# Optimization experiments

Hardware: AMD Instinct MI355X
Metric: run time of the kernel (lower is better)

## Reference

```python
import jax, jax.numpy as jnp
import numpy as np

B, T, D, V, SPK = 8, 4096, 512, 1024, 512
DECAY = 0.95
COARSE_SCALE = 0.2
RES_SCALE = 0.35
MAX_LS = 1.2
MAX_SIL = 0.35
COLD_RUNS = 2.0
MIN_DUR = 2.0


def gelu(x):
    return jax.nn.gelu(x, approximate=False)


def setup_inputs() -> dict:
    key = jax.random.key(0)
    ks = jax.random.split(key, 24)
    def n(k, shape, s=1.0):
        return jax.random.normal(k, shape, dtype=jnp.float32) * s
    inp = {}
    inp['content_units'] = jax.random.randint(ks[0], (B, T), 0, V)
    inp['log_anchor'] = n(ks[1], (B, T), 0.5) + 1.0
    inp['unit_mask'] = jax.random.randint(ks[2], (B, T), 0, 2)
    inp['sealed_mask'] = jax.random.randint(ks[3], (B, T), 0, 2)
    inp['silence_mask'] = jax.random.randint(ks[4], (B, T), 0, 2)
    inp['sep_hint'] = jax.random.uniform(ks[5], (B, T), dtype=jnp.float32)
    inp['edge_cue'] = jax.random.uniform(ks[6], (B, T), dtype=jnp.float32)
    inp['run_stability'] = jax.random.uniform(ks[7], (B, T), dtype=jnp.float32)
    inp['global_rate'] = n(ks[8], (B,), 0.1) + 1.0
    inp['local_rate_ema'] = n(ks[9], (B, 1), 0.1) + 1.0
    inp['spk_embed'] = n(ks[10], (B, SPK))
    s = 0.02
    inp['emb_table'] = n(ks[11], (V, D), s)
    inp['feat_W'] = n(ks[12], (5, D), s)      # scalar features -> dim
    inp['feat_b'] = jnp.zeros((D,), jnp.float32)
    inp['spk_W'] = n(ks[13], (SPK, D), s)
    inp['spk_b'] = jnp.zeros((D,), jnp.float32)
    inp['coarse_W1'] = n(ks[14], (D + 1, D), s)
    inp['coarse_b1'] = jnp.zeros((D,), jnp.float32)
    inp['coarse_W2'] = n(ks[15], (D, 1), s)
    inp['coarse_b2'] = jnp.zeros((1,), jnp.float32)
    inp['res_W1'] = n(ks[16], (2 * D + 1, D), s)
    inp['res_b1'] = jnp.zeros((D,), jnp.float32)
    inp['res_W2'] = n(ks[17], (D, 1), s)
    inp['res_b2'] = jnp.zeros((1,), jnp.float32)
    inp['src_rate_init'] = jnp.zeros((1,), jnp.float32)
    return inp


def _local_rate_scan(observed_log, speech_mask, init_rate):
    # Causal masked exponential-decay recurrence: emitted rate at t is the
    # state BEFORE observing step t (strictly causal); state only updates on
    # speech-commit steps.
    def step(rate, xs):
        obs, m = xs  # [B], [B]
        new = jnp.where(m > 0, DECAY * rate + (1.0 - DECAY) * obs, rate)
        return new, rate
    final, seq = jax.lax.scan(step, init_rate, (observed_log.T, speech_mask.T))
    return seq.T, final[:, None]  # [B,T], [B,1]


def reference(content_units, log_anchor, unit_mask, sealed_mask, silence_mask,
              sep_hint, edge_cue, run_stability, global_rate, local_rate_ema,
              spk_embed, emb_table, feat_W, feat_b, spk_W, spk_b,
              coarse_W1, coarse_b1, coarse_W2, coarse_b2,
              res_W1, res_b1, res_W2, res_b2, src_rate_init):
    f32 = jnp.float32
    mask = jnp.clip(unit_mask.astype(f32), 0.0, 1.0)
    sealed = jnp.clip(sealed_mask.astype(f32), 0.0, 1.0)
    silence = jnp.clip(silence_mask.astype(f32), 0.0, 1.0) * mask
    stability = jnp.clip(run_stability.astype(f32), 0.0, 1.0) * mask
    commit = mask * sealed
    sil_commit = commit * silence
    speech = commit * (1.0 - silence)

    la = log_anchor.astype(f32)
    rate_seq, rate_final = _local_rate_scan(la, speech, local_rate_ema[:, 0].astype(f32))

    # CausalUnitRunEncoder: token embedding + projection of per-step scalars
    feats = jnp.stack([la, rate_seq, silence, sep_hint.astype(f32), edge_cue.astype(f32)], axis=-1)  # [B,T,5]
    query = gelu(emb_table[content_units] + feats @ feat_W + feat_b) * mask[..., None]  # [B,T,D]

    grc = global_rate.astype(f32).reshape(-1, 1)[:, :1]  # [B,1]
    spk_ctx = jnp.tanh(spk_embed.astype(f32) @ spk_W + spk_b)  # [B,D]

    gsa = (grc - rate_seq) * commit  # global_shift_analytic [B,T]
    coarse_in = jnp.concatenate([spk_ctx, grc], axis=-1)  # [B,D+1]
    coarse_scalar = COARSE_SCALE * jnp.tanh((gelu(coarse_in @ coarse_W1 + coarse_b1) @ coarse_W2 + coarse_b2)[:, 0])  # [B]
    coarse_corr = coarse_scalar[:, None] * commit
    global_term = (gsa + coarse_corr) * commit

    # residual head: split first-layer weights to avoid materializing the concat
    Wq, Ws, wg = res_W1[:D], res_W1[D:2 * D], res_W1[2 * D]
    h = gelu(query @ Wq + (spk_ctx @ Ws)[:, None, :] + global_term[..., None] * wg + res_b1)  # [B,T,D]
    residual = RES_SCALE * jnp.tanh((h @ res_W2 + res_b2)[..., 0])  # [B,T]

    prefix_prev = jnp.maximum(jnp.cumsum(speech, axis=1) - speech, 0.0)
    cold_gate = jnp.clip(prefix_prev / COLD_RUNS, 0.0, 1.0)
    short_gate = jnp.clip((jnp.maximum(jnp.exp(la), 1.0) - 1.0) / max(1.0, MIN_DUR - 1.0), 0.0, 1.0)
    residual_gate = cold_gate * short_gate * stability * speech
    residual = residual * residual_gate

    pred_speech = jnp.clip(global_term + residual, -MAX_LS, MAX_LS) * speech
    pred_silence = jnp.clip(global_term, -MAX_SIL, MAX_SIL) * sil_commit
    pred = pred_speech + pred_silence  # unit_logstretch [B,T]
    return pred
```

## Files before the change

kernel.cpp:

```cpp
#include <hip/hip_runtime.h>
#include <hip/hip_bf16.h>

#define BB 8
#define TT 4096
#define DD 512
#define MM (BB*TT)
#define DECAYF 0.95f
#define OMDECAYF (1.0f - 0.95f)

typedef __attribute__((ext_vector_type(8))) short bf16x8;
typedef __attribute__((ext_vector_type(4))) float f32x4;

__device__ __forceinline__ float gelu_f(float x){
  return 0.5f * x * (1.0f + erff(x * 0.70710678118654752f));
}

__device__ __forceinline__ unsigned f2bf(float x){
  unsigned u = __float_as_uint(x);
  return (u + 0x7FFFu + ((u >> 16) & 1u)) >> 16;
}

__global__ __launch_bounds__(512) void pre_kernel(
    const float* __restrict__ spk_embed, const float* __restrict__ spk_W,
    const float* __restrict__ spk_b, const float* __restrict__ rW1,
    const float* __restrict__ la_g, const int* __restrict__ um,
    const int* __restrict__ sm, const int* __restrict__ zm,
    const float* __restrict__ stab_g, const float* __restrict__ lre,
    float* __restrict__ spk_ctx, unsigned short* __restrict__ wqt,
    float* __restrict__ rate_seq, float* __restrict__ rgate_a,
    int* __restrict__ active_list, int* __restrict__ acount)
{
  __shared__ float se[DD];
  __shared__ float red[8][64];
  __shared__ float tile[64][65];
  __shared__ float wAg[8], wBg[8], wSg[8];
  __shared__ int wcnt[8];
  int blk = blockIdx.x, t = threadIdx.x;
  int lane = t & 63, wid = t >> 6;

  if (blk < 64){
    int b = blk >> 3, d0 = (blk & 7) * 64;
    int dl = lane, ks = wid;
    se[t] = spk_embed[b*DD + t];
    __syncthreads();
    float a = 0.f;
    const float* wp = spk_W + (long)(ks*64)*DD + d0 + dl;
    #pragma unroll 8
    for (int k = 0; k < 64; ++k) a += se[ks*64 + k] * wp[(long)k*DD];
    red[ks][dl] = a;
    __syncthreads();
    if (t < 64){
      float s = spk_b[d0 + t];
      #pragma unroll
      for (int i = 0; i < 8; ++i) s += red[i][t];
      spk_ctx[b*DD + d0 + t] = tanhf(s);
    }
    return;
  }
  if (blk < 128){
    int tb = blk - 64;
    int nb = (tb & 7) * 64, kb = (tb >> 3) * 64;
    int tx = t & 63, ty = t >> 6;
    #pragma unroll
    for (int i = 0; i < 8; ++i){
      int k = ty + i*8;
      tile[k][tx] = rW1[(long)(kb + k)*DD + nb + tx];
    }
    __syncthreads();
    #pragma unroll
    for (int i = 0; i < 8; ++i){
      int nl = ty + i*8;
      wqt[(long)(nb + nl)*DD + kb + tx] = (unsigned short)f2bf(tile[tx][nl]);
    }
    return;
  }

  int b = blk - 128;
  int base = b*TT + t*8;
  float4 la0 = *(const float4*)(la_g + base);
  float4 la1 = *(const float4*)(la_g + base + 4);
  int4 u0 = *(const int4*)(um + base), u1 = *(const int4*)(um + base + 4);
  int4 s0 = *(const int4*)(sm + base), s1 = *(const int4*)(sm + base + 4);
  int4 z0 = *(const int4*)(zm + base), z1 = *(const int4*)(zm + base + 4);
  float4 st0 = *(const float4*)(stab_g + base), st1 = *(const float4*)(stab_g + base + 4);
  float lav[8] = {la0.x,la0.y,la0.z,la0.w,la1.x,la1.y,la1.z,la1.w};
  int uv[8] = {u0.x,u0.y,u0.z,u0.w,u1.x,u1.y,u1.z,u1.w};
  int sv[8] = {s0.x,s0.y,s0.z,s0.w,s1.x,s1.y,s1.z,s1.w};
  int zv[8] = {z0.x,z0.y,z0.z,z0.w,z1.x,z1.y,z1.z,z1.w};
  float stv_[8] = {st0.x,st0.y,st0.z,st0.w,st1.x,st1.y,st1.z,st1.w};
  float spv[8], stv[8];

  float A = 1.f, Bv = 0.f, S = 0.f;
  #pragma unroll
  for (int i = 0; i < 8; ++i){
    float m = uv[i] > 0 ? 1.f : 0.f;
    float sealed = sv[i] > 0 ? 1.f : 0.f;
    float sil = (zv[i] > 0 ? 1.f : 0.f) * m;
    float speech = (m * sealed) * (1.f - sil);
    spv[i] = speech;
    stv[i] = fminf(fmaxf(stv_[i], 0.f), 1.f) * m;
    if (speech > 0.f){
      Bv = DECAYF*Bv + OMDECAYF*lav[i];
      A *= DECAYF;
      S += 1.f;
    }
  }
  #pragma unroll
  for (int d = 1; d < 64; d <<= 1){
    float Au = __shfl_up(A, d, 64);
    float Bu = __shfl_up(Bv, d, 64);
    float Su = __shfl_up(S, d, 64);
    if (lane >= d){ Bv = A*Bu + Bv; A = A*Au; S += Su; }
  }
  if (lane == 63){ wAg[wid] = A; wBg[wid] = Bv; wSg[wid] = S; }
  float Ale = __shfl_up(A, 1, 64), Ble = __shfl_up(Bv, 1, 64), Sle = __shfl_up(S, 1, 64);
  if (lane == 0){ Ale = 1.f; Ble = 0.f; Sle = 0.f; }
  __syncthreads();
  float Awp = 1.f, Bwp = 0.f, Swp = 0.f;
  for (int w = 0; w < wid; ++w){
    Bwp = wAg[w]*Bwp + wBg[w];
    Awp = wAg[w]*Awp;
    Swp += wSg[w];
  }
  float Bex = Ale*Bwp + Ble;
  float Aex = Ale*Awp;
  float Sex = Swp + Sle;

  float rate = Aex*lre[b] + Bex;
  float ps = Sex;
  float ro[8], rg[8];
  #pragma unroll
  for (int i = 0; i < 8; ++i){
    ro[i] = rate;
    float cold = fminf(ps * 0.5f, 1.f);
    float shortg = fminf(fmaxf(expf(lav[i]) - 1.f, 0.f), 1.f);
    rg[i] = cold * shortg * stv[i] * spv[i];
    if (spv[i] > 0.f){
      rate = DECAYF*rate + OMDECAYF*lav[i];
      ps += 1.f;
    }
  }
  *(float4*)(rate_seq + base)     = make_float4(ro[0],ro[1],ro[2],ro[3]);
  *(float4*)(rate_seq + base + 4) = make_float4(ro[4],ro[5],ro[6],ro[7]);
  *(float4*)(rgate_a + base)      = make_float4(rg[0],rg[1],rg[2],rg[3]);
  *(float4*)(rgate_a + base + 4)  = make_float4(rg[4],rg[5],rg[6],rg[7]);

  int nact = 0;
  #pragma unroll
  for (int i = 0; i < 8; ++i) nact += (rg[i] != 0.f) ? 1 : 0;
  int inc = nact;
  #pragma unroll
  for (int d = 1; d < 64; d <<= 1){
    int u = __shfl_up(inc, d, 64);
    if (lane >= d) inc += u;
  }
  int myex = inc - nact;
  if (lane == 63) wcnt[wid] = inc;
  __syncthreads();
  int wbase = 0;
  for (int w = 0; w < wid; ++w) wbase += wcnt[w];
  int pos = wbase + myex;
  int* alist = active_list + b*TT;
  #pragma unroll
  for (int i = 0; i < 8; ++i){
    if (rg[i] != 0.f) alist[pos++] = base + i;
  }
  if (t == 0){
    int total = 0;
    #pragma unroll
    for (int w = 0; w < 8; ++w) total += wcnt[w];
    acount[b] = total;
  }
}

__global__ __launch_bounds__(512) void prep2_kernel(
    const float* __restrict__ spk_ctx, const float* __restrict__ rW1,
    const float* __restrict__ cW1, const float* __restrict__ cb1,
    const float* __restrict__ cW2, const float* __restrict__ grate,
    float* __restrict__ s_vec, float* __restrict__ coarse_part)
{
  __shared__ float sc[DD];
  __shared__ float red1[8][64];
  __shared__ float red2[8][64];
  int blk = blockIdx.x;
  int b = blk >> 3, d0 = (blk & 7) * 64;
  int t = threadIdx.x, dl = t & 63, ks = t >> 6;
  sc[t] = spk_ctx[b*DD + t];
  __syncthreads();
  float a1 = 0.f, a2 = 0.f;
  const float* wsp = rW1 + (long)(DD + ks*64)*DD + d0 + dl;
  const float* wcp = cW1 + (long)(ks*64)*DD + d0 + dl;
  #pragma unroll 4
  for (int k = 0; k < 64; ++k){
    float s = sc[ks*64 + k];
    a1 += s * wsp[(long)k*DD];
    a2 += s * wcp[(long)k*DD];
  }
  red1[ks][dl] = a1; red2[ks][dl] = a2;
  __syncthreads();
  if (t < 64){
    int d = d0 + t;
    float s1 = 0.f;
    float s2 = cb1[d] + grate[b] * cW1[(long)DD*DD + d];
    #pragma unroll
    for (int i = 0; i < 8; ++i){ s1 += red1[i][t]; s2 += red2[i][t]; }
    s_vec[b*DD + d] = s1;
    float hv = gelu_f(s2) * cW2[d];
    #pragma unroll
    for (int sh = 1; sh < 64; sh <<= 1) hv += __shfl_xor(hv, sh, 64);
    if (t == 0) coarse_part[blk] = hv;
  }
}

__global__ __launch_bounds__(512) void main_kernel(
    const int* __restrict__ content, const float* __restrict__ la_g,
    const float* __restrict__ sep, const float* __restrict__ edge,
    const float* __restrict__ emb, const float* __restrict__ fW,
    const float* __restrict__ fb, const float* __restrict__ rate_seq,
    const unsigned short* __restrict__ wqt,
    const float* __restrict__ s_vec, const float* __restrict__ rW1,
    const float* __restrict__ rb1, const float* __restrict__ rW2,
    const float* __restrict__ rb2, const float* __restrict__ grate,
    const float* __restrict__ coarse_part, const float* __restrict__ cb2,
    const int* __restrict__ um, const int* __restrict__ sm,
    const int* __restrict__ zm,
    const float* __restrict__ rgate_a, const int* __restrict__ active_list,
    const int* __restrict__ acount, float* __restrict__ out)
{
  __shared__ unsigned short Af[16*32*32];
  __shared__ unsigned short Bs[2][512*32];
  __shared__ float part[8][32];
  __shared__ int seg_sh[3];
  int blk = blockIdx.x, tid = threadIdx.x, wid = tid >> 6, lane = tid & 63;

  if (tid < 128){
    int gr = blk*128 + tid;
    float rgv = rgate_a[gr];
    if (rgv == 0.f){
      int b = gr >> 12;
      float csum = cb2[0];
      #pragma unroll
      for (int c = 0; c < 8; ++c) csum += coarse_part[b*8 + c];
      float cs = 0.2f * tanhf(csum);
      float m = um[gr] > 0 ? 1.f : 0.f;
      float sealed = sm[gr] > 0 ? 1.f : 0.f;
      float sil = (zm[gr] > 0 ? 1.f : 0.f) * m;
      float commit = m * sealed;
      float speech = commit * (1.f - sil);
      float silc = commit * sil;
      float g = (grate[b] - rate_seq[gr] + cs) * commit;
      out[gr] = fminf(fmaxf(g, -1.2f), 1.2f) * speech
              + fminf(fmaxf(g, -0.35f), 0.35f) * silc;
    }
  }

  const char* wbase = (const char*)wqt;
  auto stageB = [&](unsigned short* dstbuf, int kc){
    int k0b = kc * 64;
    #pragma unroll
    for (int i = 0; i < 4; ++i){
      int j = wid*4 + i;
      int n = j*16 + (lane >> 2);
      int slot = (lane & 3) ^ ((n >> 1) & 3);
      const char* src = wbase + (long)n*1024 + k0b + slot*16;
      char* dst = (char*)dstbuf + j*1024 + (lane << 4);
      __builtin_amdgcn_global_load_lds(
          (const __attribute__((address_space(1))) void*)src,
          (__attribute__((address_space(3))) void*)dst, 16, 0, 0);
    }
  };

  for (int p = blk; ; p += 256){
    if (tid == 0){
      int cum = 0, sb = -1, slo = 0, scnt = 0;
      #pragma unroll
      for (int b = 0; b < BB; ++b){
        int c = acount[b];
        int nb = (c + 31) >> 5;
        if (sb < 0 && p < cum + nb){ sb = b; slo = (p - cum) * 32; scnt = c; }
        cum += nb;
      }
      seg_sh[0] = sb; seg_sh[1] = slo; seg_sh[2] = scnt;
    }
    __syncthreads();
    int seg_b = seg_sh[0], seg_lo = seg_sh[1], seg_cnt = seg_sh[2];
    if (seg_b < 0) break;
    const int* alist = active_list + seg_b*TT;

    float csum = cb2[0];
    #pragma unroll
    for (int c = 0; c < 8; ++c) csum += coarse_part[seg_b*8 + c];
    float cs = 0.2f * tanhf(csum);
    float grc = grate[seg_b];

    stageB(&Bs[0][0], 0);

    {
      int rr = tid >> 4, kc = tid & 15;
      int q = seg_lo + rr; if (q > seg_cnt-1) q = seg_cnt-1;
      int gr = alist[q];
      float la = la_g[gr], rate = rate_seq[gr];
      float sepv = sep[gr], edgev = edge[gr];
      int k0 = kc * 32;
      const float* er = emb + (long)content[gr]*DD + k0;
      int c = (rr >> 1) & 3;
      char* abase = (char*)Af + kc*2048 + rr*64;
      #pragma unroll
      for (int s2 = 0; s2 < 4; ++s2){
        int kk = k0 + s2*8;
        float4 e0 = *(const float4*)(er + s2*8);
        float4 e1 = *(const float4*)(er + s2*8 + 4);
        float4 w00 = *(const float4*)(fW + kk);
        float4 w01 = *(const float4*)(fW + kk + 4);
        float4 w10 = *(const float4*)(fW + DD + kk);
        float4 w11 = *(const float4*)(fW + DD + kk + 4);
        float4 w30 = *(const float4*)(fW + 3*DD + kk);
        float4 w31 = *(const float4*)(fW + 3*DD + kk + 4);
        float4 w40 = *(const float4*)(fW + 4*DD + kk);
        float4 w41 = *(const float4*)(fW + 4*DD + kk + 4);
        float4 b0 = *(const float4*)(fb + kk);
        float4 b1 = *(const float4*)(fb + kk + 4);
        unsigned v0 = f2bf(gelu_f(e0.x + la*w00.x + rate*w10.x + sepv*w30.x + edgev*w40.x + b0.x));
        unsigned v1 = f2bf(gelu_f(e0.y + la*w00.y + rate*w10.y + sepv*w30.y + edgev*w40.y + b0.y));
        unsigned v2 = f2bf(gelu_f(e0.z + la*w00.z + rate*w10.z + sepv*w30.z + edgev*w40.z + b0.z));
        unsigned v3 = f2bf(gelu_f(e0.w + la*w00.w + rate*w10.w + sepv*w30.w + edgev*w40.w + b0.w));
        unsigned v4 = f2bf(gelu_f(e1.x + la*w01.x + rate*w11.x + sepv*w31.x + edgev*w41.x + b1.x));
        unsigned v5 = f2bf(gelu_f(e1.y + la*w01.y + rate*w11.y + sepv*w31.y + edgev*w41.y + b1.y));
        unsigned v6 = f2bf(gelu_f(e1.z + la*w01.z + rate*w11.z + sepv*w31.z + edgev*w41.z + b1.z));
        unsigned v7 = f2bf(gelu_f(e1.w + la*w01.w + rate*w11.w + sepv*w31.w + edgev*w41.w + b1.w));
        int4 pkv = make_int4((int)((v1 << 16) | v0), (int)((v3 << 16) | v2),
                             (int)((v5 << 16) | v4), (int)((v7 << 16) | v6));
        *(int4*)(abase + ((s2 ^ c) << 4)) = pkv;
      }
    }
    __syncthreads();

    f32x4 acc[2][4];
    #pragma unroll
    for (int i = 0; i < 2; ++i)
      #pragma unroll
      for (int j = 0; j < 4; ++j) acc[i][j] = (f32x4){0.f,0.f,0.f,0.f};

    int rgp = lane >> 4, li = lane & 15;
    #pragma unroll
    for (int kc = 0; kc < 16; ++kc){
      if (kc < 15) stageB(&Bs[(kc+1)&1][0], kc+1);
      if (kc < 15) asm volatile("s_waitcnt vmcnt(4)" ::: "memory");
      else         asm volatile("s_waitcnt vmcnt(0)" ::: "memory");
      const char* bsb = (const char*)&Bs[kc&1][0];
      bf16x8 a[2], bb[4];
      #pragma unroll
      for (int mt = 0; mt < 2; ++mt){
        int row = mt*16 + li;
        int slot = rgp ^ ((row >> 1) & 3);
        a[mt] = *(const bf16x8*)((const char*)Af + kc*2048 + row*64 + (slot << 4));
      }
      #pragma unroll
      for (int nt = 0; nt < 4; ++nt){
        int n = wid*64 + nt*16 + li;
        int slot = rgp ^ ((n >> 1) & 3);
        bb[nt] = *(const bf16x8*)(bsb + n*64 + slot*16);
      }
      #pragma unroll
      for (int mt = 0; mt < 2; ++mt)
        #pragma unroll
        for (int nt = 0; nt < 4; ++nt)
          acc[mt][nt] = __builtin_amdgcn_mfma_f32_16x16x32_bf16(a[mt], bb[nt], acc[mt][nt], 0, 0, 0);
    }

    float svv[4], wgv[4], b1v[4], w2v[4];
    #pragma unroll
    for (int nt = 0; nt < 4; ++nt){
      int j = wid*64 + nt*16 + li;
      svv[nt] = s_vec[seg_b*DD + j];
      wgv[nt] = rW1[1024*DD + j];
      b1v[nt] = rb1[j];
      w2v[nt] = rW2[j];
    }
    #pragma unroll
    for (int mt = 0; mt < 2; ++mt){
      #pragma unroll
      for (int r = 0; r < 4; ++r){
        int row = mt*16 + rgp*4 + r;
        int q = seg_lo + row; if (q > seg_cnt-1) q = seg_cnt-1;
        int gr = alist[q];
        float gt = grc - rate_seq[gr] + cs;
        float s = 0.f;
        #pragma unroll
        for (int nt = 0; nt < 4; ++nt){
          float y = acc[mt][nt][r] + svv[nt] + gt*wgv[nt] + b1v[nt];
          s += gelu_f(y) * w2v[nt];
        }
        s += __shfl_xor(s, 1, 64);
        s += __shfl_xor(s, 2, 64);
        s += __shfl_xor(s, 4, 64);
        s += __shfl_xor(s, 8, 64);
        if (li == 0) part[wid][row] = s;
      }
    }
    __syncthreads();
    if (tid < 32){
      int q = seg_lo + tid;
      if (q < seg_cnt){
        int gr = alist[q];
        float s = 0.f;
        #pragma unroll
        for (int w = 0; w < 8; ++w) s += part[w][tid];
        float resid = 0.35f * tanhf(s + rb2[0]) * rgate_a[gr];
        float g = grc - rate_seq[gr] + cs;
        out[gr] = fminf(fmaxf(g + resid, -1.2f), 1.2f);
      }
    }
    __syncthreads();
  }
}

extern "C" void kernel_launch(void* const* d_in, const int* in_sizes, int n_in,
                              void* d_out, int out_size, void* d_ws, size_t ws_size,
                              hipStream_t stream)
{
  const int*   content = (const int*)  d_in[0];
  const float* la      = (const float*)d_in[1];
  const int*   um      = (const int*)  d_in[2];
  const int*   smk     = (const int*)  d_in[3];
  const int*   zm      = (const int*)  d_in[4];
  const float* sep     = (const float*)d_in[5];
  const float* edge    = (const float*)d_in[6];
  const float* stab    = (const float*)d_in[7];
  const float* grate   = (const float*)d_in[8];
  const float* lre     = (const float*)d_in[9];
  const float* spk_e   = (const float*)d_in[10];
  const float* emb     = (const float*)d_in[11];
  const float* fW      = (const float*)d_in[12];
  const float* fb      = (const float*)d_in[13];
  const float* spk_W   = (const float*)d_in[14];
  const float* spk_b   = (const float*)d_in[15];
  const float* cW1     = (const float*)d_in[16];
  const float* cb1     = (const float*)d_in[17];
  const float* cW2     = (const float*)d_in[18];
  const float* cb2     = (const float*)d_in[19];
  const float* rW1     = (const float*)d_in[20];
  const float* rb1     = (const float*)d_in[21];
  const float* rW2     = (const float*)d_in[22];
  const float* rb2     = (const float*)d_in[23];

  char* w = (char*)d_ws;
  unsigned short* wsWqT = (unsigned short*)(w);
  size_t off = 524288;
  float* rate_seq = (float*)(w + off); off += MM*4;
  float* rgate_a  = (float*)(w + off); off += MM*4;
  int*   active_list = (int*)(w + off); off += MM*4;
  float* s_vec    = (float*)(w + off); off += BB*DD*4;
  float* spk_ctx  = (float*)(w + off); off += BB*DD*4;
  float* coarse_part = (float*)(w + off); off += 64*4;
  int*   acount   = (int*)(w + off); off += 256;

  pre_kernel<<<136, 512, 0, stream>>>(spk_e, spk_W, spk_b, rW1,
      la, um, smk, zm, stab, lre,
      spk_ctx, wsWqT, rate_seq, rgate_a, active_list, acount);
  prep2_kernel<<<64, 512, 0, stream>>>(spk_ctx, rW1, cW1, cb1, cW2, grate,
                                       s_vec, coarse_part);
  main_kernel<<<256, 512, 0, stream>>>(content, la, sep, edge, emb, fW, fb,
      rate_seq, wsWqT, s_vec, rW1, rb1, rW2, rb2, grate, coarse_part, cb2,
      um, smk, zm, rgate_a, active_list, acount, (float*)d_out);
}
```

Baseline: 41.58 us.

## Precompute query activations in mid kernel and stream them into LDS via global_load_lds

Moves the embedding+feature GELU query computation out of the GEMM main kernel into the former prep2 kernel, now a 576-block mid_kernel that writes bf16 query rows for active tokens to a 32MB workspace. The main kernel then loads its A tile straight into LDS with global_load_lds and no longer does the gather and GELU in its prologue. The aim is to take the prologue latency off the GEMM blocks and spread it over more parallel blocks. The cost is an extra write and read of up to 32MB of bf16 activations through global memory.

```diff
diff --git a/kernel.cpp b/kernel.cpp
--- a/kernel.cpp
+++ b/kernel.cpp
@@ -173,50 +173,88 @@
   }
 }
 
-__global__ __launch_bounds__(512) void prep2_kernel(
+__global__ __launch_bounds__(512) void mid_kernel(
     const float* __restrict__ spk_ctx, const float* __restrict__ rW1,
     const float* __restrict__ cW1, const float* __restrict__ cb1,
     const float* __restrict__ cW2, const float* __restrict__ grate,
-    float* __restrict__ s_vec, float* __restrict__ coarse_part)
-{
-  __shared__ float sc[DD];
-  __shared__ float red1[8][64];
-  __shared__ float red2[8][64];
-  int blk = blockIdx.x;
-  int b = blk >> 3, d0 = (blk & 7) * 64;
-  int t = threadIdx.x, dl = t & 63, ks = t >> 6;
-  sc[t] = spk_ctx[b*DD + t];
-  __syncthreads();
-  float a1 = 0.f, a2 = 0.f;
-  const float* wsp = rW1 + (long)(DD + ks*64)*DD + d0 + dl;
-  const float* wcp = cW1 + (long)(ks*64)*DD + d0 + dl;
-  #pragma unroll 4
-  for (int k = 0; k < 64; ++k){
-    float s = sc[ks*64 + k];
-    a1 += s * wsp[(long)k*DD];
-    a2 += s * wcp[(long)k*DD];
-  }
-  red1[ks][dl] = a1; red2[ks][dl] = a2;
-  __syncthreads();
-  if (t < 64){
-    int d = d0 + t;
-    float s1 = 0.f;
-    float s2 = cb1[d] + grate[b] * cW1[(long)DD*DD + d];
-    #pragma unroll
-    for (int i = 0; i < 8; ++i){ s1 += red1[i][t]; s2 += red2[i][t]; }
-    s_vec[b*DD + d] = s1;
-    float hv = gelu_f(s2) * cW2[d];
-    #pragma unroll
-    for (int sh = 1; sh < 64; sh <<= 1) hv += __shfl_xor(hv, sh, 64);
-    if (t == 0) coarse_part[blk] = hv;
-  }
-}
-
-__global__ __launch_bounds__(512) void main_kernel(
     const int* __restrict__ content, const float* __restrict__ la_g,
     const float* __restrict__ sep, const float* __restrict__ edge,
     const float* __restrict__ emb, const float* __restrict__ fW,
     const float* __restrict__ fb, const float* __restrict__ rate_seq,
+    const int* __restrict__ active_list, const int* __restrict__ acount,
+    float* __restrict__ s_vec, float* __restrict__ coarse_part,
+    unsigned short* __restrict__ wsQ)
+{
+  int blk = blockIdx.x, t = threadIdx.x;
+  int lane = t & 63, wid = t >> 6;
+
+  if (blk < 64){
+    __shared__ float sc[DD];
+    __shared__ float red1[8][64];
+    __shared__ float red2[8][64];
+    int b = blk >> 3, d0 = (blk & 7) * 64;
+    int dl = lane, ks = wid;
+    sc[t] = spk_ctx[b*DD + t];
+    __syncthreads();
+    float a1 = 0.f, a2 = 0.f;
+    const float* wsp = rW1 + (long)(DD + ks*64)*DD + d0 + dl;
+    const float* wcp = cW1 + (long)(ks*64)*DD + d0 + dl;
+    #pragma unroll 4
+    for (int k = 0; k < 64; ++k){
+      float s = sc[ks*64 + k];
+      a1 += s * wsp[(long)k*DD];
+      a2 += s * wcp[(long)k*DD];
+    }
+    red1[ks][dl] = a1; red2[ks][dl] = a2;
+    __syncthreads();
+    if (t < 64){
+      int d = d0 + t;
+      float s1 = 0.f;
+      float s2 = cb1[d] + grate[b] * cW1[(long)DD*DD + d];
+      #pragma unroll
+      for (int i = 0; i < 8; ++i){ s1 += red1[i][t]; s2 += red2[i][t]; }
+      s_vec[b*DD + d] = s1;
+      float hv = gelu_f(s2) * cW2[d];
+      #pragma unroll
+      for (int sh = 1; sh < 64; sh <<= 1) hv += __shfl_xor(hv, sh, 64);
+      if (t == 0) coarse_part[blk] = hv;
+    }
+    return;
+  }
+
+  int tb = blk - 64;
+  int b = tb >> 6;
+  int slot0 = (tb & 63) * 8 + wid;
+  int cnt = acount[b];
+  const int* alist = active_list + b*TT;
+  int c0 = lane * 8;
+  for (int j = slot0; j < cnt; j += 512){
+    int gr = alist[j];
+    float la = la_g[gr], rate = rate_seq[gr];
+    float sepv = sep[gr], edgev = edge[gr];
+    const float* er = emb + (long)content[gr]*DD + c0;
+    float4 e0 = *(const float4*)(er), e1 = *(const float4*)(er + 4);
+    float4 w00 = *(const float4*)(fW + c0),        w01 = *(const float4*)(fW + c0 + 4);
+    float4 w10 = *(const float4*)(fW + DD + c0),   w11 = *(const float4*)(fW + DD + c0 + 4);
+    float4 w30 = *(const float4*)(fW + 3*DD + c0), w31 = *(const float4*)(fW + 3*DD + c0 + 4);
+    float4 w40 = *(const float4*)(fW + 4*DD + c0), w41 = *(const float4*)(fW + 4*DD + c0 + 4);
+    float4 b0 = *(const float4*)(fb + c0), b1 = *(const float4*)(fb + c0 + 4);
+    unsigned v0 = f2bf(gelu_f(e0.x + la*w00.x + rate*w10.x + sepv*w30.x + edgev*w40.x + b0.x));
+    unsigned v1 = f2bf(gelu_f(e0.y + la*w00.y + rate*w10.y + sepv*w30.y + edgev*w40.y + b0.y));
+    unsigned v2 = f2bf(gelu_f(e0.z + la*w00.z + rate*w10.z + sepv*w30.z + edgev*w40.z + b0.z));
+    unsigned v3 = f2bf(gelu_f(e0.w + la*w00.w + rate*w10.w + sepv*w30.w + edgev*w40.w + b0.w));
+    unsigned v4 = f2bf(gelu_f(e1.x + la*w01.x + rate*w11.x + sepv*w31.x + edgev*w41.x + b1.x));
+    unsigned v5 = f2bf(gelu_f(e1.y + la*w01.y + rate*w11.y + sepv*w31.y + edgev*w41.y + b1.y));
+    unsigned v6 = f2bf(gelu_f(e1.z + la*w01.z + rate*w11.z + sepv*w31.z + edgev*w41.z + b1.z));
+    unsigned v7 = f2bf(gelu_f(e1.w + la*w01.w + rate*w11.w + sepv*w31.w + edgev*w41.w + b1.w));
+    int4 pkv = make_int4((int)((v1 << 16) | v0), (int)((v3 << 16) | v2),
+                         (int)((v5 << 16) | v4), (int)((v7 << 16) | v6));
+    *(int4*)(wsQ + (long)(b*TT + j)*DD + c0) = pkv;
+  }
+}
+
+__global__ __launch_bounds__(512) void main_kernel(
+    const float* __restrict__ rate_seq, const unsigned short* __restrict__ wsQ,
     const unsigned short* __restrict__ wqt,
     const float* __restrict__ s_vec, const float* __restrict__ rW1,
     const float* __restrict__ rb1, const float* __restrict__ rW2,
@@ -286,6 +324,7 @@
     int seg_b = seg_sh[0], seg_lo = seg_sh[1], seg_cnt = seg_sh[2];
     if (seg_b < 0) break;
     const int* alist = active_list + seg_b*TT;
+    const char* qseg = (const char*)(wsQ + (long)(seg_b*TT + seg_lo)*DD);
 
     float csum = cb2[0];
     #pragma unroll
@@ -293,46 +332,20 @@
     float cs = 0.2f * tanhf(csum);
     float grc = grate[seg_b];
 
+    #pragma unroll
+    for (int i = 0; i < 4; ++i){
+      int idx = wid + i*8;
+      int kcA = idx >> 1, half = idx & 1;
+      int row = half*16 + (lane >> 2);
+      int slot = (lane & 3) ^ ((row >> 1) & 3);
+      const char* src = qseg + (long)row*1024 + kcA*64 + slot*16;
+      char* dst = (char*)Af + kcA*2048 + half*1024 + (lane << 4);
+      __builtin_amdgcn_global_load_lds(
+          (const __attribute__((address_space(1))) void*)src,
+          (__attribute__((address_space(3))) void*)dst, 16, 0, 0);
+    }
     stageB(&Bs[0][0], 0);
-
-    {
-      int rr = tid >> 4, kc = tid & 15;
-      int q = seg_lo + rr; if (q > seg_cnt-1) q = seg_cnt-1;
-      int gr = alist[q];
-      float la = la_g[gr], rate = rate_seq[gr];
-      float sepv = sep[gr], edgev = edge[gr];
-      int k0 = kc * 32;
-      const float* er = emb + (long)content[gr]*DD + k0;
-      int c = (rr >> 1) & 3;
-      char* abase = (char*)Af + kc*2048 + rr*64;
-      #pragma unroll
-      for (int s2 = 0; s2 < 4; ++s2){
-        int kk = k0 + s2*8;
-        float4 e0 = *(const float4*)(er + s2*8);
-        float4 e1 = *(const float4*)(er + s2*8 + 4);
-        float4 w00 = *(const float4*)(fW + kk);
-        float4 w01 = *(const float4*)(fW + kk + 4);
-        float4 w10 = *(const float4*)(fW + DD + kk);
-        float4 w11 = *(const float4*)(fW + DD + kk + 4);
-        float4 w30 = *(const float4*)(fW + 3*DD + kk);
-        float4 w31 = *(const float4*)(fW + 3*DD + kk + 4);
-        float4 w40 = *(const float4*)(fW + 4*DD + kk);
-        float4 w41 = *(const float4*)(fW + 4*DD + kk + 4);
-        float4 b0 = *(const float4*)(fb + kk);
-        float4 b1 = *(const float4*)(fb + kk + 4);
-        unsigned v0 = f2bf(gelu_f(e0.x + la*w00.x + rate*w10.x + sepv*w30.x + edgev*w40.x + b0.x));
-        unsigned v1 = f2bf(gelu_f(e0.y + la*w00.y + rate*w10.y + sepv*w30.y + edgev*w40.y + b0.y));
-        unsigned v2 = f2bf(gelu_f(e0.z + la*w00.z + rate*w10.z + sepv*w30.z + edgev*w40.z + b0.z));
-        unsigned v3 = f2bf(gelu_f(e0.w + la*w00.w + rate*w10.w + sepv*w30.w + edgev*w40.w + b0.w));
-        unsigned v4 = f2bf(gelu_f(e1.x + la*w01.x + rate*w11.x + sepv*w31.x + edgev*w41.x + b1.x));
-        unsigned v5 = f2bf(gelu_f(e1.y + la*w01.y + rate*w11.y + sepv*w31.y + edgev*w41.y + b1.y));
-        unsigned v6 = f2bf(gelu_f(e1.z + la*w01.z + rate*w11.z + sepv*w31.z + edgev*w41.z + b1.z));
-        unsigned v7 = f2bf(gelu_f(e1.w + la*w01.w + rate*w11.w + sepv*w31.w + edgev*w41.w + b1.w));
-        int4 pkv = make_int4((int)((v1 << 16) | v0), (int)((v3 << 16) | v2),
-                             (int)((v5 << 16) | v4), (int)((v7 << 16) | v6));
-        *(int4*)(abase + ((s2 ^ c) << 4)) = pkv;
-      }
-    }
+    asm volatile("s_waitcnt vmcnt(0)" ::: "memory");
     __syncthreads();
 
     f32x4 acc[2][4];
@@ -445,8 +458,9 @@
   const float* rb2     = (const float*)d_in[23];
 
   char* w = (char*)d_ws;
-  unsigned short* wsWqT = (unsigned short*)(w);
-  size_t off = 524288;
+  unsigned short* wsQ   = (unsigned short*)(w);
+  unsigned short* wsWqT = (unsigned short*)(w + 33554432);
+  size_t off = 33554432 + 524288;
   float* rate_seq = (float*)(w + off); off += MM*4;
   float* rgate_a  = (float*)(w + off); off += MM*4;
   int*   active_list = (int*)(w + off); off += MM*4;
@@ -458,9 +472,10 @@
   pre_kernel<<<136, 512, 0, stream>>>(spk_e, spk_W, spk_b, rW1,
       la, um, smk, zm, stab, lre,
       spk_ctx, wsWqT, rate_seq, rgate_a, active_list, acount);
-  prep2_kernel<<<64, 512, 0, stream>>>(spk_ctx, rW1, cW1, cb1, cW2, grate,
-                                       s_vec, coarse_part);
-  main_kernel<<<256, 512, 0, stream>>>(content, la, sep, edge, emb, fW, fb,
-      rate_seq, wsWqT, s_vec, rW1, rb1, rW2, rb2, grate, coarse_part, cb2,
+  mid_kernel<<<576, 512, 0, stream>>>(spk_ctx, rW1, cW1, cb1, cW2, grate,
+      content, la, sep, edge, emb, fW, fb, rate_seq, active_list, acount,
+      s_vec, coarse_part, wsQ);
+  main_kernel<<<256, 512, 0, stream>>>(rate_seq, wsQ, wsWqT,
+      s_vec, rW1, rb1, rW2, rb2, grate, coarse_part, cb2,
       um, smk, zm, rgate_a, active_list, acount, (float*)d_out);
 }
```

New measurement: 35.32 us, median of 2. 15.0% less time.
